# Optimization experiments

Hardware: AMD Instinct MI355X
Metric: run time of the kernel (lower is better)

Reference implementation:

```python
import jax, jax.numpy as jnp
import numpy as np

N = 50000        # nodes
E_RAND = 800000  # random edges (self-loops appended -> E = 850000)
H = 8            # num_heads
D = 32           # h_feat_dim
IN = 128         # in_feat_dim
SM = 256         # sm_dim
SP = 128         # sp_dim
NEG_SLOPE = 0.2  # DGL GATv2Conv default


def setup_inputs() -> dict:
    key = jax.random.key(0)
    ks = jax.random.split(key, 16)
    s = 0.05
    self_loops = jnp.arange(N, dtype=jnp.int32)
    return {
        "sm_feats": jax.random.normal(ks[0], (N, SM), jnp.float32),
        "sp_feats": jax.random.normal(ks[1], (N, SP), jnp.float32),
        "src": jnp.concatenate([jax.random.randint(ks[2], (E_RAND,), 0, N, jnp.int32), self_loops]),
        "dst": jnp.concatenate([jax.random.randint(ks[3], (E_RAND,), 0, N, jnp.int32), self_loops]),
        # T1 / T2 linears
        "T1_w": jax.random.normal(ks[4], (SM, IN), jnp.float32) * s,
        "T1_b": jnp.zeros((IN,), jnp.float32),
        "T2_w": jax.random.normal(ks[5], (SP, IN), jnp.float32) * s,
        "T2_b": jnp.zeros((IN,), jnp.float32),
        # GATv2 layer 1: in = 2*IN
        "g1_src_w": jax.random.normal(ks[6], (2 * IN, H * D), jnp.float32) * s,
        "g1_dst_w": jax.random.normal(ks[7], (2 * IN, H * D), jnp.float32) * s,
        "g1_attn": jax.random.normal(ks[8], (H, D), jnp.float32) * s,
        "g1_bias": jnp.zeros((H * D,), jnp.float32),
        # GATv2 layer 2: in = D (after head-mean)
        "g2_src_w": jax.random.normal(ks[9], (D, H * D), jnp.float32) * s,
        "g2_dst_w": jax.random.normal(ks[10], (D, H * D), jnp.float32) * s,
        "g2_attn": jax.random.normal(ks[11], (H, D), jnp.float32) * s,
        "g2_bias": jnp.zeros((H * D,), jnp.float32),
    }


def gatv2_conv(x, src, dst, w_src, w_dst, attn, bias):
    # DGL GATv2Conv (share_weights=False, bias=True, no residual/activation)
    feat_src = (x @ w_src).reshape(-1, H, D)   # [N,H,D]
    feat_dst = (x @ w_dst).reshape(-1, H, D)   # [N,H,D]
    e = jax.nn.leaky_relu(feat_src[src] + feat_dst[dst], NEG_SLOPE)  # [E,H,D]
    score = jnp.einsum('ehd,hd->eh', e, attn)  # [E,H]
    # edge softmax over incoming edges per destination (self-loops ensure non-empty)
    smax = jax.ops.segment_max(score, dst, num_segments=N)           # [N,H]
    ex = jnp.exp(score - smax[dst])
    denom = jax.ops.segment_sum(ex, dst, num_segments=N)             # [N,H]
    alpha = ex / denom[dst]                                          # [E,H]
    out = jax.ops.segment_sum(alpha[:, :, None] * feat_src[src], dst, num_segments=N)  # [N,H,D]
    return out + bias.reshape(1, H, D)


def reference(sm_feats, sp_feats, src, dst,
              T1_w, T1_b, T2_w, T2_b,
              g1_src_w, g1_dst_w, g1_attn, g1_bias,
              g2_src_w, g2_dst_w, g2_attn, g2_bias):
    in_feat = jnp.concatenate([sm_feats @ T1_w + T1_b,
                               sp_feats @ T2_w + T2_b], axis=1)      # [N, 2*IN]
    h = gatv2_conv(in_feat, src, dst, g1_src_w, g1_dst_w, g1_attn, g1_bias)
    h = jax.nn.elu(h).mean(axis=1)                                   # [N, D]
    h = gatv2_conv(h, src, dst, g2_src_w, g2_dst_w, g2_attn, g2_bias)
    return h.mean(axis=1)                                            # [N, D]
```

## Files before the change

kernel.cpp:

```cpp
#include <hip/hip_runtime.h>
#include <hip/hip_fp16.h>


typedef unsigned int uint32;
typedef unsigned short u16;
typedef float f32x4 __attribute__((ext_vector_type(4)));
typedef _Float16 f16x2 __attribute__((ext_vector_type(2)));
typedef _Float16 f16x8 __attribute__((ext_vector_type(8)));

union H2 { f16x2 v; uint32 u; };

__device__ __forceinline__ int wave_incl_scan(int x) {
  int lane = threadIdx.x & 63;
#pragma unroll
  for (int off = 1; off < 64; off <<= 1) {
    int t = __shfl_up(x, off, 64);
    if (lane >= off) x += t;
  }
  return x;
}

__global__ __launch_bounds__(256) void k_deg(const int* __restrict__ dst, int* __restrict__ deg, int E) {
  int e = blockIdx.x * 256 + threadIdx.x;
  if (e < E) atomicAdd(&deg[dst[e]], 1);
}

__global__ __launch_bounds__(256) void k_blkscan(const int* __restrict__ in, int* __restrict__ out,
                                                 int* __restrict__ blksum, int n) {
  __shared__ int wsum[4];
  int tid = threadIdx.x;
  int i0 = blockIdx.x * 1024 + tid * 4;
  int v0 = 0, v1 = 0, v2 = 0, v3 = 0;
  if (i0 + 3 < n) {
    int4 t = *(const int4*)(in + i0);
    v0 = t.x; v1 = t.y; v2 = t.z; v3 = t.w;
  } else {
    if (i0 < n) v0 = in[i0];
    if (i0 + 1 < n) v1 = in[i0 + 1];
    if (i0 + 2 < n) v2 = in[i0 + 2];
    if (i0 + 3 < n) v3 = in[i0 + 3];
  }
  int ts = v0 + v1 + v2 + v3;
  int incl = wave_incl_scan(ts);
  int lane = tid & 63, wid = tid >> 6;
  if (lane == 63) wsum[wid] = incl;
  __syncthreads();
  if (tid == 0) {
    int a = wsum[0], b = wsum[1], c = wsum[2], d = wsum[3];
    wsum[0] = 0; wsum[1] = a; wsum[2] = a + b; wsum[3] = a + b + c;
    blksum[blockIdx.x] = a + b + c + d;
  }
  __syncthreads();
  int excl = wsum[wid] + incl - ts;
  if (i0 + 3 < n) {
    int4 o; o.x = excl; o.y = excl + v0; o.z = excl + v0 + v1; o.w = excl + v0 + v1 + v2;
    *(int4*)(out + i0) = o;
  } else {
    if (i0 < n) out[i0] = excl;
    if (i0 + 1 < n) out[i0 + 1] = excl + v0;
    if (i0 + 2 < n) out[i0 + 2] = excl + v0 + v1;
    if (i0 + 3 < n) out[i0 + 3] = excl + v0 + v1 + v2;
  }
}

__global__ void k_scan_top(int* __restrict__ bs, int G) {
  int lane = threadIdx.x;
  int base = 0;
  for (int s = 0; s < G; s += 64) {
    int i = s + lane;
    int v = (i < G) ? bs[i] : 0;
    int incl = wave_incl_scan(v);
    if (i < G) bs[i] = base + incl - v;
    base += __shfl(incl, 63, 64);
  }
}

__global__ __launch_bounds__(256) void k_addoff(int* __restrict__ rp, const int* __restrict__ bs, int n, int Etot) {
  int i = blockIdx.x * 256 + threadIdx.x;
  if (i < n) rp[i] += bs[i >> 10];
  if (i == 0) rp[n] = Etot;
}

__global__ __launch_bounds__(256) void k_fill(const int* __restrict__ src, const int* __restrict__ dst,
                                              const int* __restrict__ rp, int* __restrict__ cnt,
                                              int* __restrict__ csr_src, int E) {
  int e = blockIdx.x * 256 + threadIdx.x;
  if (e < E) {
    int d = dst[e];
    int p = rp[d] + atomicAdd(&cnt[d], 1);
    csr_src[p] = src[e];
  }
}

__global__ __launch_bounds__(256) void k_precomb(const float* __restrict__ T1w, const float* __restrict__ T1b,
                                                 const float* __restrict__ T2w, const float* __restrict__ T2b,
                                                 const float* __restrict__ G1, const float* __restrict__ G2,
                                                 __half* __restrict__ Bf, float* __restrict__ cvec) {
  int bb = blockIdx.x;
  const float* G = (bb < 385) ? G1 : G2;
  int off = (bb < 385) ? 0 : 256;
  int r = (bb < 385) ? bb : bb - 385;
  int j = threadIdx.x;
  float acc = 0.f;
  if (r < 256) {
    for (int m = 0; m < 128; m++) acc += T1w[r * 128 + m] * G[m * 256 + j];
  } else if (r < 384) {
    int rr = r - 256;
    for (int m = 0; m < 128; m++) acc += T2w[rr * 128 + m] * G[(128 + m) * 256 + j];
  } else {
    for (int m = 0; m < 128; m++) acc += T1b[m] * G[m * 256 + j] + T2b[m] * G[(128 + m) * 256 + j];
    cvec[off + j] = acc;
    return;
  }
  int k = r, colabs = off + j;
  int kt = k >> 5, lq = (k >> 3) & 3, j8 = k & 7;
  int cb = colabs >> 7, colr = colabs & 127, ni = colr >> 4, lr = colr & 15;
  size_t idx = ((size_t)(((cb * 12 + kt) * 8 + ni) * 4 + lq) * 16 + lr) * 8 + j8;
  Bf[idx] = __float2half(acc);
}

#define GLL(GP, LP)                                                     \
  __builtin_amdgcn_global_load_lds(                                     \
      (const __attribute__((address_space(1))) void*)(GP),              \
      (__attribute__((address_space(3))) void*)(LP), 16, 0, 0)

__global__ __launch_bounds__(256, 4) void k_gemm(const float* __restrict__ sm, const float* __restrict__ sp,
                                                 const u16* __restrict__ Bf, const float* __restrict__ cvec,
                                                 __half* __restrict__ fs, __half* __restrict__ fd, int N) {
  __shared__ u16 BFl[3 * 4096];
  int tid = threadIdx.x, w = tid >> 6, l = tid & 63;
  int lr = l & 15, lq = l >> 4;
  int L = blockIdx.x;
  int x = L & 7, m = L >> 3;
  int cb = m & 3;
  int rb = x + 8 * (m >> 2);
  int col0 = cb * 128, row0 = rb * 128;
  if (row0 >= N) return;
  int r0 = row0 + w * 32 + lr;
  int r1 = r0 + 16;
  int c0 = r0 < N ? r0 : N - 1;
  int c1 = r1 < N ? r1 : N - 1;
  const float* psm0 = sm + (size_t)c0 * 256 + lq * 8;
  const float* psm1 = sm + (size_t)c1 * 256 + lq * 8;
  const float* psp0 = sp + (size_t)c0 * 128 + lq * 8;
  const float* psp1 = sp + (size_t)c1 * 128 + lq * 8;

  f32x4 acc[2][8];
#pragma unroll
  for (int mt = 0; mt < 2; mt++)
#pragma unroll
    for (int ni = 0; ni < 8; ni++) acc[mt][ni] = (f32x4){0.f, 0.f, 0.f, 0.f};

#define STAGE_B(S, BUF)                                                 \
  {                                                                     \
    size_t g0 = (size_t)(cb * 12 + (S)) * 4096;                         \
    _Pragma("unroll") for (int i = 0; i < 2; i++) {                     \
      int c = i * 256 + tid;                                            \
      int lb = (BUF)*4096 + (i * 4 + w) * 512;                          \
      GLL(Bf + g0 + (size_t)c * 8, &BFl[lb]);                           \
    }                                                                   \
  }

#define LOADA(P, D)                                                     \
  {                                                                     \
    const float* _g0 = ((P) < 8) ? (psm0 + (P)*32) : (psp0 + ((P)-8) * 32); \
    const float* _g1 = ((P) < 8) ? (psm1 + (P)*32) : (psp1 + ((P)-8) * 32); \
    D[0] = *(const float4*)_g0;                                         \
    D[1] = *(const float4*)(_g0 + 4);                                   \
    D[2] = *(const float4*)_g1;                                         \
    D[3] = *(const float4*)(_g1 + 4);                                   \
  }

  float4 Aa[4], Ab[4];
  LOADA(0, Aa);
  STAGE_B(0, 0);
  STAGE_B(1, 1);
  asm volatile("s_waitcnt vmcnt(2)" ::: "memory");
  __builtin_amdgcn_sched_barrier(0);
  __builtin_amdgcn_s_barrier();

#pragma unroll
  for (int st = 0; st < 12; st++) {
    const int slot = st % 3;
    const float4* Dc = (st & 1) ? Ab : Aa;
    float4* Dn = (st & 1) ? Aa : Ab;
    if (st < 11) LOADA(st + 1, Dn);
    if (st < 10) STAGE_B(st + 2, (st + 2) % 3);
    f16x8 a0, a1;
    a0[0] = (_Float16)Dc[0].x; a0[1] = (_Float16)Dc[0].y;
    a0[2] = (_Float16)Dc[0].z; a0[3] = (_Float16)Dc[0].w;
    a0[4] = (_Float16)Dc[1].x; a0[5] = (_Float16)Dc[1].y;
    a0[6] = (_Float16)Dc[1].z; a0[7] = (_Float16)Dc[1].w;
    a1[0] = (_Float16)Dc[2].x; a1[1] = (_Float16)Dc[2].y;
    a1[2] = (_Float16)Dc[2].z; a1[3] = (_Float16)Dc[2].w;
    a1[4] = (_Float16)Dc[3].x; a1[5] = (_Float16)Dc[3].y;
    a1[6] = (_Float16)Dc[3].z; a1[7] = (_Float16)Dc[3].w;
#pragma unroll
    for (int ni = 0; ni < 8; ni++) {
      int lo = slot * 4096 + (ni * 64 + l) * 8;
      f16x8 bf = *(const f16x8*)&BFl[lo];
      acc[0][ni] = __builtin_amdgcn_mfma_f32_16x16x32_f16(a0, bf, acc[0][ni], 0, 0, 0);
      acc[1][ni] = __builtin_amdgcn_mfma_f32_16x16x32_f16(a1, bf, acc[1][ni], 0, 0, 0);
    }
    if (st < 10) {
      asm volatile("s_waitcnt vmcnt(6)" ::: "memory");
    } else if (st == 10) {
      asm volatile("s_waitcnt vmcnt(4)" ::: "memory");
    }
    if (st < 11) {
      __builtin_amdgcn_sched_barrier(0);
      __builtin_amdgcn_s_barrier();
    }
  }

#pragma unroll
  for (int mt = 0; mt < 2; mt++) {
    int rbr = row0 + w * 32 + mt * 16 + lq * 4;
#pragma unroll
    for (int ni = 0; ni < 8; ni++) {
      int c = col0 + ni * 16 + lr;
      float cv = cvec[c];
      __half* op = fs; int cc = c;
      if (c >= 256) { op = fd; cc = c - 256; }
#pragma unroll
      for (int r = 0; r < 4; r++) {
        int rr = rbr + r;
        if (rr < N) op[(size_t)rr * 256 + cc] = __float2half(acc[mt][ni][r] + cv);
      }
    }
  }
#undef STAGE_B
#undef LOADA
}

__global__ __launch_bounds__(256) void k_feat2(const float* __restrict__ h, const float* __restrict__ Ws,
                                               const float* __restrict__ Wd, __half* __restrict__ fs,
                                               __half* __restrict__ fd, int N) {
  int j = threadIdx.x;
  int n0 = blockIdx.x * 32;
  float ws[32], wd[32];
#pragma unroll
  for (int k = 0; k < 32; k++) {
    ws[k] = Ws[k * 256 + j];
    wd[k] = Wd[k * 256 + j];
  }
  int nend = n0 + 32; if (nend > N) nend = N;
#pragma unroll 2
  for (int n = n0; n < nend; n++) {
    const float* hr = h + (size_t)n * 32;
    float as = 0.f, ad = 0.f;
#pragma unroll
    for (int k = 0; k < 32; k++) {
      float hv = hr[k];
      as += hv * ws[k];
      ad += hv * wd[k];
    }
    fs[(size_t)n * 256 + j] = __float2half(as);
    fd[(size_t)n * 256 + j] = __float2half(ad);
  }
}

template <int FINAL>
__global__ __launch_bounds__(256) void k_edge(const uint2* __restrict__ fs, const uint2* __restrict__ fd,
                                              const int* __restrict__ csr_src, const int* __restrict__ rp,
                                              const float* __restrict__ attn, const float* __restrict__ bias,
                                              float* __restrict__ out, int N) {
  int n = blockIdx.x * 4 + (threadIdx.x >> 6);
  if (n >= N) return;
  int lane = threadIdx.x & 63;
  float4 av = ((const float4*)attn)[lane];
  H2 AV01, AV23, Y01, Y23;
  AV01.v = (f16x2){(_Float16)av.x, (_Float16)av.y};
  AV23.v = (f16x2){(_Float16)av.z, (_Float16)av.w};
  const f16x2 c02 = {(_Float16)0.2f, (_Float16)0.2f};
  uint2 yu = fd[(size_t)n * 64 + lane];
  Y01.u = yu.x; Y23.u = yu.y;
  int beg = rp[n], end = rp[n + 1];
  float den0 = 0.f, den1 = 0.f;
  float4 acc0 = {0.f, 0.f, 0.f, 0.f}, acc1 = {0.f, 0.f, 0.f, 0.f};

  auto edge1 = [&](uint2 xu, float& den, float4& acc) {
    H2 Xa, Xb; Xa.u = xu.x; Xb.u = xu.y;
    f16x2 ea = Xa.v + Y01.v, eb = Xb.v + Y23.v;
    f16x2 ta = __builtin_elementwise_max(ea, ea * c02);
    f16x2 tb = __builtin_elementwise_max(eb, eb * c02);
    float p = __builtin_amdgcn_fdot2(ta, AV01.v, 0.f, false);
    p = __builtin_amdgcn_fdot2(tb, AV23.v, p, false);
    p += __shfl_xor(p, 1, 64);
    p += __shfl_xor(p, 2, 64);
    p += __shfl_xor(p, 4, 64);
    float wgt = __expf(p);
    den += wgt;
    acc.x += wgt * (float)Xa.v.x; acc.y += wgt * (float)Xa.v.y;
    acc.z += wgt * (float)Xb.v.x; acc.w += wgt * (float)Xb.v.y;
  };

  int e = beg;
  int nq = (end - beg) >> 2;
  if (nq > 0) {
    int s0 = csr_src[e], s1 = csr_src[e + 1], s2 = csr_src[e + 2], s3 = csr_src[e + 3];
    uint2 x0 = fs[(size_t)s0 * 64 + lane];
    uint2 x1 = fs[(size_t)s1 * 64 + lane];
    uint2 x2 = fs[(size_t)s2 * 64 + lane];
    uint2 x3 = fs[(size_t)s3 * 64 + lane];
    for (int q = 1; q < nq; q++) {
      int b2 = e + 4 * q;
      int t0 = csr_src[b2], t1 = csr_src[b2 + 1], t2 = csr_src[b2 + 2], t3 = csr_src[b2 + 3];
      uint2 y0 = fs[(size_t)t0 * 64 + lane];
      uint2 y1 = fs[(size_t)t1 * 64 + lane];
      uint2 y2 = fs[(size_t)t2 * 64 + lane];
      uint2 y3 = fs[(size_t)t3 * 64 + lane];
      edge1(x0, den0, acc0); edge1(x1, den1, acc1);
      edge1(x2, den0, acc0); edge1(x3, den1, acc1);
      x0 = y0; x1 = y1; x2 = y2; x3 = y3;
    }
    edge1(x0, den0, acc0); edge1(x1, den1, acc1);
    edge1(x2, den0, acc0); edge1(x3, den1, acc1);
    e += 4 * nq;
  }
  for (; e < end; e++) {
    int s0 = csr_src[e];
    uint2 xu = fs[(size_t)s0 * 64 + lane];
    edge1(xu, den0, acc0);
  }

  float4 acc = {acc0.x + acc1.x, acc0.y + acc1.y, acc0.z + acc1.z, acc0.w + acc1.w};
  float invd = 1.f / (den0 + den1);
  float4 b = ((const float4*)bias)[lane];
  acc.x = acc.x * invd + b.x;
  acc.y = acc.y * invd + b.y;
  acc.z = acc.z * invd + b.z;
  acc.w = acc.w * invd + b.w;
  if (!FINAL) {
    acc.x = acc.x > 0.f ? acc.x : expm1f(acc.x);
    acc.y = acc.y > 0.f ? acc.y : expm1f(acc.y);
    acc.z = acc.z > 0.f ? acc.z : expm1f(acc.z);
    acc.w = acc.w > 0.f ? acc.w : expm1f(acc.w);
  }
#pragma unroll
  for (int mask = 8; mask <= 32; mask <<= 1) {
    acc.x += __shfl_xor(acc.x, mask, 64);
    acc.y += __shfl_xor(acc.y, mask, 64);
    acc.z += __shfl_xor(acc.z, mask, 64);
    acc.w += __shfl_xor(acc.w, mask, 64);
  }
  if (lane < 8) {
    float4 o = {acc.x * 0.125f, acc.y * 0.125f, acc.z * 0.125f, acc.w * 0.125f};
    ((float4*)out)[(size_t)n * 8 + lane] = o;
  }
}

extern "C" void kernel_launch(void* const* d_in, const int* in_sizes, int n_in,
                              void* d_out, int out_size, void* d_ws, size_t ws_size,
                              hipStream_t stream) {
  const float* sm  = (const float*)d_in[0];
  const float* sp  = (const float*)d_in[1];
  const int*   src = (const int*)d_in[2];
  const int*   dst = (const int*)d_in[3];
  const float* T1w = (const float*)d_in[4];
  const float* T1b = (const float*)d_in[5];
  const float* T2w = (const float*)d_in[6];
  const float* T2b = (const float*)d_in[7];
  const float* g1sw = (const float*)d_in[8];
  const float* g1dw = (const float*)d_in[9];
  const float* g1a  = (const float*)d_in[10];
  const float* g1b  = (const float*)d_in[11];
  const float* g2sw = (const float*)d_in[12];
  const float* g2dw = (const float*)d_in[13];
  const float* g2a  = (const float*)d_in[14];
  const float* g2b  = (const float*)d_in[15];
  const int N = in_sizes[1] / 128;
  const int E = in_sizes[2];
  float* out = (float*)d_out;

  size_t off = 0;
  char* wsb = (char*)d_ws;
  auto alloc = [&](size_t bytes) -> void* {
    void* p = wsb + off;
    off += (bytes + 255) & ~(size_t)255;
    return p;
  };
  __half* Bf  = (__half*)alloc((size_t)512 * 384 * 2);
  float* cvec  = (float*)alloc(512 * 4);
  int* deg     = (int*)alloc((size_t)N * 4);
  int* cnt     = (int*)alloc((size_t)N * 4);
  int* row_ptr = (int*)alloc((size_t)(N + 1) * 4);
  int* blksum  = (int*)alloc(4096 * 4);
  int* csr_src = (int*)alloc((size_t)E * 4);
  __half* fs   = (__half*)alloc((size_t)N * 256 * 2);
  __half* fd   = (__half*)alloc((size_t)N * 256 * 2);
  float* hmid  = (float*)alloc((size_t)N * 32 * 4);
  (void)ws_size; (void)n_in; (void)out_size;

  (void)hipMemsetAsync(deg, 0, (size_t)N * 4, stream);
  (void)hipMemsetAsync(cnt, 0, (size_t)N * 4, stream);

  k_deg<<<(E + 255) / 256, 256, 0, stream>>>(dst, deg, E);
  int nblk = (N + 1023) / 1024;
  k_blkscan<<<nblk, 256, 0, stream>>>(deg, row_ptr, blksum, N);
  k_scan_top<<<1, 64, 0, stream>>>(blksum, nblk);
  k_addoff<<<(N + 255) / 256, 256, 0, stream>>>(row_ptr, blksum, N, E);
  k_fill<<<(E + 255) / 256, 256, 0, stream>>>(src, dst, row_ptr, cnt, csr_src, E);

  k_precomb<<<770, 256, 0, stream>>>(T1w, T1b, T2w, T2b, g1sw, g1dw, Bf, cvec);

  int rbs = (N + 127) / 128;
  int rbp = (rbs + 7) & ~7;
  k_gemm<<<dim3(rbp * 4), 256, 0, stream>>>(sm, sp, (const u16*)Bf, cvec, fs, fd, N);
  k_edge<0><<<(N + 3) / 4, 256, 0, stream>>>((const uint2*)fs, (const uint2*)fd, csr_src, row_ptr, g1a, g1b, hmid, N);

  k_feat2<<<(N + 31) / 32, 256, 0, stream>>>(hmid, g2sw, g2dw, fs, fd, N);
  k_edge<1><<<(N + 3) / 4, 256, 0, stream>>>((const uint2*)fs, (const uint2*)fd, csr_src, row_ptr, g2a, g2b, out, N);
}
```

Baseline: 462.0 us.

## Process two edges per wave with 16-byte loads per lane in edge kernel

The edge aggregation kernel now splits each 64-lane wave into two halves. Each half handles a different incoming edge and each lane loads 8 fp16 features (uint4) instead of 4. This halves the number of serial edge iterations per destination node and widens the gather loads. The cost is a cross-half reduction at the end, masking on odd-degree tails, more accumulator registers, and a shallower software prefetch (one pair ahead instead of four edges).

```diff
diff --git a/kernel.cpp b/kernel.cpp
--- a/kernel.cpp
+++ b/kernel.cpp
@@ -261,92 +261,97 @@
 }
 
 template <int FINAL>
-__global__ __launch_bounds__(256) void k_edge(const uint2* __restrict__ fs, const uint2* __restrict__ fd,
+__global__ __launch_bounds__(256) void k_edge(const uint4* __restrict__ fs4, const uint4* __restrict__ fd4,
                                               const int* __restrict__ csr_src, const int* __restrict__ rp,
                                               const float* __restrict__ attn, const float* __restrict__ bias,
                                               float* __restrict__ out, int N) {
   int n = blockIdx.x * 4 + (threadIdx.x >> 6);
   if (n >= N) return;
   int lane = threadIdx.x & 63;
-  float4 av = ((const float4*)attn)[lane];
-  H2 AV01, AV23, Y01, Y23;
-  AV01.v = (f16x2){(_Float16)av.x, (_Float16)av.y};
-  AV23.v = (f16x2){(_Float16)av.z, (_Float16)av.w};
+  int lh = lane & 31;
+  float4 a0 = ((const float4*)attn)[lh * 2];
+  float4 a1 = ((const float4*)attn)[lh * 2 + 1];
+  H2 AV01, AV23, AV45, AV67;
+  AV01.v = (f16x2){(_Float16)a0.x, (_Float16)a0.y};
+  AV23.v = (f16x2){(_Float16)a0.z, (_Float16)a0.w};
+  AV45.v = (f16x2){(_Float16)a1.x, (_Float16)a1.y};
+  AV67.v = (f16x2){(_Float16)a1.z, (_Float16)a1.w};
   const f16x2 c02 = {(_Float16)0.2f, (_Float16)0.2f};
-  uint2 yu = fd[(size_t)n * 64 + lane];
-  Y01.u = yu.x; Y23.u = yu.y;
+  uint4 yu = fd4[(size_t)n * 32 + lh];
+  H2 Y01, Y23, Y45, Y67;
+  Y01.u = yu.x; Y23.u = yu.y; Y45.u = yu.z; Y67.u = yu.w;
   int beg = rp[n], end = rp[n + 1];
-  float den0 = 0.f, den1 = 0.f;
-  float4 acc0 = {0.f, 0.f, 0.f, 0.f}, acc1 = {0.f, 0.f, 0.f, 0.f};
-
-  auto edge1 = [&](uint2 xu, float& den, float4& acc) {
-    H2 Xa, Xb; Xa.u = xu.x; Xb.u = xu.y;
-    f16x2 ea = Xa.v + Y01.v, eb = Xb.v + Y23.v;
-    f16x2 ta = __builtin_elementwise_max(ea, ea * c02);
-    f16x2 tb = __builtin_elementwise_max(eb, eb * c02);
-    float p = __builtin_amdgcn_fdot2(ta, AV01.v, 0.f, false);
-    p = __builtin_amdgcn_fdot2(tb, AV23.v, p, false);
+  float den = 0.f;
+  float acc[8] = {0.f, 0.f, 0.f, 0.f, 0.f, 0.f, 0.f, 0.f};
+
+  auto pair1 = [&](uint4 xu, bool tail) {
+    H2 Xa, Xb, Xc, Xd;
+    Xa.u = xu.x; Xb.u = xu.y; Xc.u = xu.z; Xd.u = xu.w;
+    f16x2 e0 = Xa.v + Y01.v, e1 = Xb.v + Y23.v, e2 = Xc.v + Y45.v, e3 = Xd.v + Y67.v;
+    f16x2 t0 = __builtin_elementwise_max(e0, e0 * c02);
+    f16x2 t1 = __builtin_elementwise_max(e1, e1 * c02);
+    f16x2 t2 = __builtin_elementwise_max(e2, e2 * c02);
+    f16x2 t3 = __builtin_elementwise_max(e3, e3 * c02);
+    float p = __builtin_amdgcn_fdot2(t0, AV01.v, 0.f, false);
+    p = __builtin_amdgcn_fdot2(t1, AV23.v, p, false);
+    p = __builtin_amdgcn_fdot2(t2, AV45.v, p, false);
+    p = __builtin_amdgcn_fdot2(t3, AV67.v, p, false);
     p += __shfl_xor(p, 1, 64);
     p += __shfl_xor(p, 2, 64);
-    p += __shfl_xor(p, 4, 64);
     float wgt = __expf(p);
+    if (tail && lane >= 32) wgt = 0.f;
     den += wgt;
-    acc.x += wgt * (float)Xa.v.x; acc.y += wgt * (float)Xa.v.y;
-    acc.z += wgt * (float)Xb.v.x; acc.w += wgt * (float)Xb.v.y;
+    acc[0] += wgt * (float)Xa.v.x; acc[1] += wgt * (float)Xa.v.y;
+    acc[2] += wgt * (float)Xb.v.x; acc[3] += wgt * (float)Xb.v.y;
+    acc[4] += wgt * (float)Xc.v.x; acc[5] += wgt * (float)Xc.v.y;
+    acc[6] += wgt * (float)Xd.v.x; acc[7] += wgt * (float)Xd.v.y;
   };
 
   int e = beg;
-  int nq = (end - beg) >> 2;
-  if (nq > 0) {
-    int s0 = csr_src[e], s1 = csr_src[e + 1], s2 = csr_src[e + 2], s3 = csr_src[e + 3];
-    uint2 x0 = fs[(size_t)s0 * 64 + lane];
-    uint2 x1 = fs[(size_t)s1 * 64 + lane];
-    uint2 x2 = fs[(size_t)s2 * 64 + lane];
-    uint2 x3 = fs[(size_t)s3 * 64 + lane];
-    for (int q = 1; q < nq; q++) {
-      int b2 = e + 4 * q;
-      int t0 = csr_src[b2], t1 = csr_src[b2 + 1], t2 = csr_src[b2 + 2], t3 = csr_src[b2 + 3];
-      uint2 y0 = fs[(size_t)t0 * 64 + lane];
-      uint2 y1 = fs[(size_t)t1 * 64 + lane];
-      uint2 y2 = fs[(size_t)t2 * 64 + lane];
-      uint2 y3 = fs[(size_t)t3 * 64 + lane];
-      edge1(x0, den0, acc0); edge1(x1, den1, acc1);
-      edge1(x2, den0, acc0); edge1(x3, den1, acc1);
-      x0 = y0; x1 = y1; x2 = y2; x3 = y3;
-    }
-    edge1(x0, den0, acc0); edge1(x1, den1, acc1);
-    edge1(x2, den0, acc0); edge1(x3, den1, acc1);
-    e += 4 * nq;
-  }
-  for (; e < end; e++) {
-    int s0 = csr_src[e];
-    uint2 xu = fs[(size_t)s0 * 64 + lane];
-    edge1(xu, den0, acc0);
-  }
-
-  float4 acc = {acc0.x + acc1.x, acc0.y + acc1.y, acc0.z + acc1.z, acc0.w + acc1.w};
-  float invd = 1.f / (den0 + den1);
-  float4 b = ((const float4*)bias)[lane];
-  acc.x = acc.x * invd + b.x;
-  acc.y = acc.y * invd + b.y;
-  acc.z = acc.z * invd + b.z;
-  acc.w = acc.w * invd + b.w;
-  if (!FINAL) {
-    acc.x = acc.x > 0.f ? acc.x : expm1f(acc.x);
-    acc.y = acc.y > 0.f ? acc.y : expm1f(acc.y);
-    acc.z = acc.z > 0.f ? acc.z : expm1f(acc.z);
-    acc.w = acc.w > 0.f ? acc.w : expm1f(acc.w);
-  }
-#pragma unroll
-  for (int mask = 8; mask <= 32; mask <<= 1) {
-    acc.x += __shfl_xor(acc.x, mask, 64);
-    acc.y += __shfl_xor(acc.y, mask, 64);
-    acc.z += __shfl_xor(acc.z, mask, 64);
-    acc.w += __shfl_xor(acc.w, mask, 64);
-  }
-  if (lane < 8) {
-    float4 o = {acc.x * 0.125f, acc.y * 0.125f, acc.z * 0.125f, acc.w * 0.125f};
-    ((float4*)out)[(size_t)n * 8 + lane] = o;
+  int np = (end - beg) >> 1;
+  if (np > 0) {
+    int sA = csr_src[e], sB = csr_src[e + 1];
+    int s = (lane < 32) ? sA : sB;
+    uint4 xcur = fs4[(size_t)s * 32 + lh];
+    for (int q = 1; q < np; q++) {
+      int eb = e + 2 * q;
+      int tA = csr_src[eb], tB = csr_src[eb + 1];
+      int t = (lane < 32) ? tA : tB;
+      uint4 xnext = fs4[(size_t)t * 32 + lh];
+      pair1(xcur, false);
+      xcur = xnext;
+    }
+    pair1(xcur, false);
+    e += 2 * np;
+  }
+  if (e < end) {
+    int sA = csr_src[e];
+    uint4 xu = fs4[(size_t)sA * 32 + lh];
+    pair1(xu, true);
+  }
+
+  den += __shfl_xor(den, 32, 64);
+#pragma unroll
+  for (int j = 0; j < 8; j++) acc[j] += __shfl_xor(acc[j], 32, 64);
+  float invd = 1.f / den;
+  float4 b0 = ((const float4*)bias)[lh * 2];
+  float4 b1 = ((const float4*)bias)[lh * 2 + 1];
+  float bj[8] = {b0.x, b0.y, b0.z, b0.w, b1.x, b1.y, b1.z, b1.w};
+#pragma unroll
+  for (int j = 0; j < 8; j++) {
+    float v = acc[j] * invd + bj[j];
+    if (!FINAL) v = v > 0.f ? v : expm1f(v);
+    acc[j] = v;
+  }
+#pragma unroll
+  for (int mask = 4; mask <= 16; mask <<= 1)
+#pragma unroll
+    for (int j = 0; j < 8; j++) acc[j] += __shfl_xor(acc[j], mask, 64);
+  if (lane < 4) {
+    float4 o0 = {acc[0] * 0.125f, acc[1] * 0.125f, acc[2] * 0.125f, acc[3] * 0.125f};
+    float4 o1 = {acc[4] * 0.125f, acc[5] * 0.125f, acc[6] * 0.125f, acc[7] * 0.125f};
+    ((float4*)out)[(size_t)n * 8 + lane * 2] = o0;
+    ((float4*)out)[(size_t)n * 8 + lane * 2 + 1] = o1;
   }
 }
 
@@ -407,8 +412,8 @@
   int rbs = (N + 127) / 128;
   int rbp = (rbs + 7) & ~7;
   k_gemm<<<dim3(rbp * 4), 256, 0, stream>>>(sm, sp, (const u16*)Bf, cvec, fs, fd, N);
-  k_edge<0><<<(N + 3) / 4, 256, 0, stream>>>((const uint2*)fs, (const uint2*)fd, csr_src, row_ptr, g1a, g1b, hmid, N);
+  k_edge<0><<<(N + 3) / 4, 256, 0, stream>>>((const uint4*)fs, (const uint4*)fd, csr_src, row_ptr, g1a, g1b, hmid, N);
 
   k_feat2<<<(N + 31) / 32, 256, 0, stream>>>(hmid, g2sw, g2dw, fs, fd, N);
-  k_edge<1><<<(N + 3) / 4, 256, 0, stream>>>((const uint2*)fs, (const uint2*)fd, csr_src, row_ptr, g2a, g2b, out, N);
-}
+  k_edge<1><<<(N + 3) / 4, 256, 0, stream>>>((const uint4*)fs, (const uint4*)fd, csr_src, row_ptr, g2a, g2b, out, N);
+}
```

Result: no change. 456.5 us (-1.2%).
